# Optimization experiments

Hardware: AMD Instinct MI355X
Metric: run time of the kernel (lower is better)

## Reference

```python
import jax, jax.numpy as jnp
import numpy as np

DIM = 512
N_HEADS = 8
HEAD_DIM = DIM // N_HEADS
HID = 4 * DIM
N_LEVELS = 3  # len(chunk_sizes)
EPS = 1e-5


def layernorm(x, w, b):
    mu = jnp.mean(x, axis=-1, keepdims=True)
    var = jnp.var(x, axis=-1, keepdims=True)
    return (x - mu) * jax.lax.rsqrt(var + EPS) * w + b


def setup_inputs() -> dict:
    key = jax.random.key(0)
    ks = jax.random.split(key, 12)
    s = 1.0 / np.sqrt(DIM)
    sh = 1.0 / np.sqrt(HID)
    inp = {
        "x": jax.random.normal(ks[0], (4, 2048, DIM), dtype=jnp.float32),
        # torch nn.Linear stores weight as [out, in]; y = x @ W.T
        "Wq": jax.random.uniform(ks[1], (DIM, DIM), minval=-s, maxval=s),
        "Wk": jax.random.uniform(ks[2], (DIM, DIM), minval=-s, maxval=s),
        "Wv": jax.random.uniform(ks[3], (DIM, DIM), minval=-s, maxval=s),
        "Wo": jax.random.uniform(ks[4], (DIM, DIM), minval=-s, maxval=s),
        "ln1_w": jnp.ones((DIM,)), "ln1_b": jnp.zeros((DIM,)),
        "ln2_w": jnp.ones((DIM,)), "ln2_b": jnp.zeros((DIM,)),
        # CMS: per-level MLP, stored as [L, in, out]
        "cms_W1": jax.random.uniform(ks[5], (N_LEVELS, DIM, HID), minval=-s, maxval=s),
        "cms_b1": jnp.zeros((N_LEVELS, HID)),
        "cms_W2": jax.random.uniform(ks[6], (N_LEVELS, HID, DIM), minval=-sh, maxval=sh),
        "cms_b2": jnp.zeros((N_LEVELS, DIM)),
    }
    return inp


def self_mod_attn(h, Wq, Wk, Wv, Wo):
    B, S, _ = h.shape
    def split(y):  # [B,S,dim] -> [B,H,S,D]
        return y.reshape(B, S, N_HEADS, HEAD_DIM).transpose(0, 2, 1, 3)
    Q = split(h @ Wq.T)
    K = split(h @ Wk.T)
    V = split(h @ Wv.T)
    # per-step memory delta, mean over batch: U[h,s,d,k] = mean_b v_t k_t^T
    U = jnp.einsum("bhsd,bhsk->hsdk", V, K) / B
    # memory starts at zero (buffer) and accumulates INCLUDING step t before readout
    M = jnp.cumsum(U, axis=1)  # [H,S,D,D]
    y = jnp.einsum("hsdk,bhsk->bhsd", M, Q)  # readout
    y = y.transpose(0, 2, 1, 3).reshape(B, S, DIM)
    return y @ Wo.T


def cms(h, cms_W1, cms_b1, cms_W2, cms_b2):
    # sequential chain of per-level MLPs (dim -> 4*dim -> dim)
    for l in range(N_LEVELS):
        h = jax.nn.gelu(h @ cms_W1[l] + cms_b1[l]) @ cms_W2[l] + cms_b2[l]
    return h


def reference(x, Wq, Wk, Wv, Wo, ln1_w, ln1_b, ln2_w, ln2_b,
              cms_W1, cms_b1, cms_W2, cms_b2):
    x = x + self_mod_attn(layernorm(x, ln1_w, ln1_b), Wq, Wk, Wv, Wo)
    x = x + cms(layernorm(x, ln2_w, ln2_b), cms_W1, cms_b1, cms_W2, cms_b2)
    return x
```

## Files before the change

kernel.cpp:

```cpp
#include <hip/hip_runtime.h>
#include <hip/hip_bf16.h>
#include <cstdint>
#include <cstddef>

typedef __attribute__((ext_vector_type(8))) short bf16x8;
typedef __attribute__((ext_vector_type(4))) float f32x4;

#define MFMA16(a, b, c) __builtin_amdgcn_mfma_f32_16x16x32_bf16((a), (b), (c), 0, 0, 0)

static __device__ __forceinline__ unsigned short f2bf(float f) {
    union { float f; unsigned u; } v; v.f = f;
    unsigned r = v.u + 0x7fffu + ((v.u >> 16) & 1u);
    return (unsigned short)(r >> 16);
}

static __device__ __forceinline__ float bf2f(unsigned short u) {
    union { unsigned u; float f; } v; v.u = ((unsigned)u) << 16; return v.f;
}

static __device__ __forceinline__ float gelu_tanh(float x) {
    float z = 0.7978845608028654f * (x + 0.044715f * x * x * x);
    float a = fabsf(z);
    float e = __expf(-2.0f * a);
    float t = (1.0f - e) / (1.0f + e);
    t = (z < 0.0f) ? -t : t;
    return 0.5f * x * (1.0f + t);
}

static __device__ __forceinline__ void gload16(const void* g, void* l) {
    __builtin_amdgcn_global_load_lds((const __attribute__((address_space(1))) unsigned int*)g,
                                     (__attribute__((address_space(3))) unsigned int*)l,
                                     16, 0, 0);
}

__global__ __launch_bounds__(256) void wcvt_kernel(const float* __restrict__ a, const float* __restrict__ b,
                                                   const float* __restrict__ c, const float* __restrict__ d,
                                                   unsigned short* __restrict__ o) {
    int i = blockIdx.x * 256 + threadIdx.x;
    int idx = i * 4;
    int which = idx >> 18;
    int off = idx & 262143;
    const float* src = (which == 0) ? a : (which == 1) ? b : (which == 2) ? c : d;
    float4 v = *(const float4*)(src + off);
    unsigned long long p = (unsigned long long)f2bf(v.x) | ((unsigned long long)f2bf(v.y) << 16)
                         | ((unsigned long long)f2bf(v.z) << 32) | ((unsigned long long)f2bf(v.w) << 48);
    *(unsigned long long*)(o + idx) = p;
}

__global__ __launch_bounds__(256) void wtrans_kernel(const float* __restrict__ in, unsigned short* __restrict__ out,
                                                     int R, int C) {
    __shared__ float tile[32][33];
    size_t lvl = blockIdx.z;
    in  += lvl * (size_t)R * C;
    out += lvl * (size_t)R * C;
    int c0 = blockIdx.x * 32, r0 = blockIdx.y * 32;
    int tx = threadIdx.x & 31, ty = threadIdx.x >> 5;
    #pragma unroll
    for (int ii = 0; ii < 4; ++ii) {
        int i = ty * 4 + ii;
        tile[i][tx] = in[(size_t)(r0 + i) * C + c0 + tx];
    }
    __syncthreads();
    #pragma unroll
    for (int jj = 0; jj < 4; ++jj) {
        int j = ty * 4 + jj;
        out[(size_t)(c0 + j) * R + r0 + tx] = f2bf(tile[tx][j]);
    }
}

__global__ __launch_bounds__(256) void ln_kernel(const float* __restrict__ x,
                                                 const float* __restrict__ w,
                                                 const float* __restrict__ b,
                                                 unsigned short* __restrict__ out) {
    int tid = threadIdx.x, l = tid & 63, wv = tid >> 6;
    size_t row = (size_t)blockIdx.x * 4 + wv;
    const float* xr = x + row * 512 + l * 8;
    float4 v0 = *(const float4*)xr;
    float4 v1 = *(const float4*)(xr + 4);
    float vv[8] = {v0.x, v0.y, v0.z, v0.w, v1.x, v1.y, v1.z, v1.w};
    float s = 0.f, q = 0.f;
    #pragma unroll
    for (int j = 0; j < 8; ++j) { s += vv[j]; q += vv[j] * vv[j]; }
    #pragma unroll
    for (int off = 1; off < 64; off <<= 1) { s += __shfl_xor(s, off); q += __shfl_xor(q, off); }
    float mu = s * (1.0f / 512.0f);
    float rs = rsqrtf(q * (1.0f / 512.0f) - mu * mu + 1e-5f);
    union { unsigned short us[8]; uint4 u; } pk;
    #pragma unroll
    for (int j = 0; j < 8; ++j)
        pk.us[j] = f2bf((vv[j] - mu) * rs * w[l * 8 + j] + b[l * 8 + j]);
    *(uint4*)(out + row * 512 + l * 8) = pk.u;
}

template<int EPI>
__global__ __launch_bounds__(512, 2) void gemm256(
    const unsigned short* __restrict__ A,
    const unsigned short* __restrict__ Bt,
    int K, int lda, int ldb, int N,
    unsigned short* __restrict__ outb,
    const float* __restrict__ bias,
    size_t planeStride) {
    __shared__ bf16x8 As[2][2048];
    __shared__ bf16x8 Bs[2][2048];
    const int tid = threadIdx.x, l = tid & 63, w = tid >> 6;
    const int m0 = blockIdx.x * 256, n0 = blockIdx.y * 256;
    const int wr = (w >> 2) * 128, wc = (w & 3) * 64;
    const int srow = l >> 3;
    const int scol = ((l & 7) ^ srow) * 8;

    if constexpr (EPI == 5) {
        size_t z = blockIdx.z;
        A    += z * (size_t)K;
        Bt   += z * (size_t)K;
        outb += z * planeStride;
    }

    const int nkt = K >> 6;
    auto stage = [&](int buf, int kt) {
        const unsigned short* Ag = A + (size_t)m0 * lda + kt * 64;
        const unsigned short* Bg = Bt + (size_t)n0 * ldb + kt * 64;
        #pragma unroll
        for (int i = 0; i < 4; ++i) {
            int chunk = i * 8 + w;
            int row = chunk * 8 + srow;
            gload16(Ag + (size_t)row * lda + scol, &As[buf][chunk * 64]);
            gload16(Bg + (size_t)row * ldb + scol, &Bs[buf][chunk * 64]);
        }
    };

    f32x4 acc[8][4] = {};
    stage(0, 0);
    __syncthreads();
    int cur = 0;
    for (int kt = 0; kt < nkt; ++kt) {
        if (kt + 1 < nkt) stage(cur ^ 1, kt + 1);
        #pragma unroll
        for (int kk = 0; kk < 2; ++kk) {
            bf16x8 af[8], bfr[4];
            #pragma unroll
            for (int mi = 0; mi < 8; ++mi) {
                int r = wr + mi * 16 + (l & 15);
                af[mi] = As[cur][r * 8 + ((kk * 4 + (l >> 4)) ^ (r & 7))];
            }
            #pragma unroll
            for (int ni = 0; ni < 4; ++ni) {
                int r = wc + ni * 16 + (l & 15);
                bfr[ni] = Bs[cur][r * 8 + ((kk * 4 + (l >> 4)) ^ (r & 7))];
            }
            #pragma unroll
            for (int mi = 0; mi < 8; ++mi)
                #pragma unroll
                for (int ni = 0; ni < 4; ++ni)
                    acc[mi][ni] = MFMA16(af[mi], bfr[ni], acc[mi][ni]);
        }
        __syncthreads();
        cur ^= 1;
    }

    #pragma unroll
    for (int mi = 0; mi < 8; ++mi)
        #pragma unroll
        for (int ni = 0; ni < 4; ++ni) {
            int col = n0 + wc + ni * 16 + (l & 15);
            #pragma unroll
            for (int r = 0; r < 4; ++r) {
                int row = m0 + wr + mi * 16 + (l >> 4) * 4 + r;
                float v = acc[mi][ni][r];
                size_t idx = (size_t)row * N + col;
                if constexpr (EPI == 0) {
                    outb[idx] = f2bf(v);
                } else if constexpr (EPI == 2) {
                    v += bias[col];
                    outb[idx] = f2bf(gelu_tanh(v));
                } else {
                    outb[idx] = f2bf(v);
                }
            }
        }
}

template<int EPI, int TN>
__global__ __launch_bounds__(256) void gemm_bt(
    const unsigned short* __restrict__ A,
    const unsigned short* __restrict__ Bt,
    int K, int lda, int ldb, int N,
    unsigned short* __restrict__ outb,
    float* __restrict__ outf,
    const float* __restrict__ bias,
    const float* __restrict__ resid) {
    constexpr int NI = TN / 32;
    constexpr int BCH = TN / 32;
    __shared__ bf16x8 As[2][1024];
    __shared__ bf16x8 Bs[2][TN * 8];
    const int tid = threadIdx.x, l = tid & 63, w = tid >> 6;
    const int m0 = blockIdx.x * 128, n0 = blockIdx.y * TN;
    const int wr = (w >> 1) * 64, wc = (w & 1) * (TN / 2);
    const int srow = l >> 3;
    const int scol = ((l & 7) ^ srow) * 8;

    const int nkt = K >> 6;
    auto stage = [&](int buf, int kt) {
        const unsigned short* Ag = A + (size_t)m0 * lda + kt * 64;
        const unsigned short* Bg = Bt + (size_t)n0 * ldb + kt * 64;
        #pragma unroll
        for (int i = 0; i < 4; ++i) {
            int chunk = i * 4 + w;
            int row = chunk * 8 + srow;
            gload16(Ag + (size_t)row * lda + scol, &As[buf][chunk * 64]);
        }
        #pragma unroll
        for (int i = 0; i < BCH; ++i) {
            int chunk = i * 4 + w;
            int row = chunk * 8 + srow;
            gload16(Bg + (size_t)row * ldb + scol, &Bs[buf][chunk * 64]);
        }
    };

    f32x4 acc[4][NI] = {};
    stage(0, 0);
    __syncthreads();
    int cur = 0;
    for (int kt = 0; kt < nkt; ++kt) {
        if (kt + 1 < nkt) stage(cur ^ 1, kt + 1);
        #pragma unroll
        for (int kk = 0; kk < 2; ++kk) {
            bf16x8 af[4], bfr[NI];
            #pragma unroll
            for (int mi = 0; mi < 4; ++mi) {
                int r = wr + mi * 16 + (l & 15);
                af[mi] = As[cur][r * 8 + ((kk * 4 + (l >> 4)) ^ (r & 7))];
            }
            #pragma unroll
            for (int ni = 0; ni < NI; ++ni) {
                int r = wc + ni * 16 + (l & 15);
                bfr[ni] = Bs[cur][r * 8 + ((kk * 4 + (l >> 4)) ^ (r & 7))];
            }
            #pragma unroll
            for (int mi = 0; mi < 4; ++mi)
                #pragma unroll
                for (int ni = 0; ni < NI; ++ni)
                    acc[mi][ni] = MFMA16(af[mi], bfr[ni], acc[mi][ni]);
        }
        __syncthreads();
        cur ^= 1;
    }

    #pragma unroll
    for (int mi = 0; mi < 4; ++mi)
        #pragma unroll
        for (int ni = 0; ni < NI; ++ni) {
            int col = n0 + wc + ni * 16 + (l & 15);
            #pragma unroll
            for (int r = 0; r < 4; ++r) {
                int row = m0 + wr + mi * 16 + (l >> 4) * 4 + r;
                float v = acc[mi][ni][r];
                size_t idx = (size_t)row * N + col;
                if constexpr (EPI == 1) {
                    outf[idx] = v + resid[idx];
                } else {
                    outb[idx] = f2bf(v);
                }
            }
        }
}

template<bool FINAL>
__global__ __launch_bounds__(256) void reduce_down(const unsigned short* __restrict__ P,
                                                   const float* __restrict__ bias,
                                                   const float* __restrict__ resid,
                                                   unsigned short* __restrict__ outb,
                                                   float* __restrict__ outf) {
    size_t i = ((size_t)blockIdx.x * 256 + threadIdx.x) * 8;
    int col = (int)(i & 511);
    bf16x8 a0 = *(const bf16x8*)(P + i);
    bf16x8 a1 = *(const bf16x8*)(P + 4194304 + i);
    bf16x8 a2 = *(const bf16x8*)(P + 2 * 4194304 + i);
    bf16x8 a3 = *(const bf16x8*)(P + 3 * 4194304 + i);
    float4 b0 = *(const float4*)(bias + col);
    float4 b1 = *(const float4*)(bias + col + 4);
    float bs[8] = {b0.x, b0.y, b0.z, b0.w, b1.x, b1.y, b1.z, b1.w};
    float v[8];
    #pragma unroll
    for (int j = 0; j < 8; ++j)
        v[j] = (bf2f((unsigned short)a0[j]) + bf2f((unsigned short)a1[j]))
             + (bf2f((unsigned short)a2[j]) + bf2f((unsigned short)a3[j])) + bs[j];
    if constexpr (FINAL) {
        const float4 r0 = *(const float4*)(resid + i);
        const float4 r1 = *(const float4*)(resid + i + 4);
        float4 o0 = {v[0] + r0.x, v[1] + r0.y, v[2] + r0.z, v[3] + r0.w};
        float4 o1 = {v[4] + r1.x, v[5] + r1.y, v[6] + r1.z, v[7] + r1.w};
        *(float4*)(outf + i) = o0;
        *(float4*)(outf + i + 4) = o1;
    } else {
        union { unsigned short us[8]; uint4 u; } pk;
        #pragma unroll
        for (int j = 0; j < 8; ++j) pk.us[j] = f2bf(v[j]);
        *(uint4*)(outb + i) = pk.u;
    }
}

__global__ __launch_bounds__(256) void attn_u_kernel(
    const unsigned short* __restrict__ QKV,
    float* __restrict__ U) {
    const int c = blockIdx.x, h = blockIdx.y;
    const int tid = threadIdx.x, l = tid & 63, w = tid >> 6;
    __shared__ __align__(16) unsigned short Kt[64 * 256];
    __shared__ __align__(16) unsigned short Vt[64 * 256];
    for (int i = 0; i < 8; ++i) {
        int idx = i * 256 + tid;
        int tr = idx >> 3, g = idx & 7;
        int bb = tr >> 6, tl = tr & 63;
        size_t go = (size_t)(bb * 2048 + c * 64 + tl) * 1536 + h * 64 + g * 8;
        bf16x8 kv = *(const bf16x8*)(QKV + go + 512);
        bf16x8 vv = *(const bf16x8*)(QKV + go + 1024);
        #pragma unroll
        for (int j = 0; j < 8; ++j) {
            int d = g * 8 + j;
            int ts = tr ^ ((d & 7) << 3);
            Kt[d * 256 + ts] = (unsigned short)kv[j];
            Vt[d * 256 + ts] = (unsigned short)vv[j];
        }
    }
    __syncthreads();
    const int dr = (w >> 1) * 32, kc = (w & 1) * 32;
    f32x4 acc[2][2] = {};
    #pragma unroll
    for (int kk = 0; kk < 8; ++kk) {
        bf16x8 av[2], bk[2];
        #pragma unroll
        for (int mi = 0; mi < 2; ++mi) {
            int r = dr + mi * 16 + (l & 15);
            av[mi] = *(const bf16x8*)&Vt[r * 256 + ((kk * 32 + (l >> 4) * 8) ^ ((r & 7) << 3))];
        }
        #pragma unroll
        for (int ni = 0; ni < 2; ++ni) {
            int r = kc + ni * 16 + (l & 15);
            bk[ni] = *(const bf16x8*)&Kt[r * 256 + ((kk * 32 + (l >> 4) * 8) ^ ((r & 7) << 3))];
        }
        #pragma unroll
        for (int mi = 0; mi < 2; ++mi)
            #pragma unroll
            for (int ni = 0; ni < 2; ++ni)
                acc[mi][ni] = MFMA16(av[mi], bk[ni], acc[mi][ni]);
    }
    float* Uo = U + (size_t)(h * 32 + c) * 4096;
    #pragma unroll
    for (int mi = 0; mi < 2; ++mi)
        #pragma unroll
        for (int ni = 0; ni < 2; ++ni)
            #pragma unroll
            for (int r = 0; r < 4; ++r) {
                int d = dr + mi * 16 + (l >> 4) * 4 + r;
                int k2 = kc + ni * 16 + (l & 15);
                Uo[d * 64 + k2] = acc[mi][ni][r] * 0.25f;
            }
}

__global__ __launch_bounds__(256) void attn_scan_kernel(const float* __restrict__ U,
                                                        unsigned short* __restrict__ Mx) {
    int e = blockIdx.x * 256 + threadIdx.x;
    int h = blockIdx.y;
    const float* Ub = U + (size_t)h * 32 * 4096 + e;
    unsigned short* Mb = Mx + (size_t)h * 32 * 4096 + e;
    float a = 0.0f;
    #pragma unroll
    for (int c0 = 0; c0 < 32; c0 += 4) {
        float u0 = Ub[(c0 + 0) * 4096];
        float u1 = Ub[(c0 + 1) * 4096];
        float u2 = Ub[(c0 + 2) * 4096];
        float u3 = Ub[(c0 + 3) * 4096];
        Mb[(c0 + 0) * 4096] = f2bf(a); a += u0;
        Mb[(c0 + 1) * 4096] = f2bf(a); a += u1;
        Mb[(c0 + 2) * 4096] = f2bf(a); a += u2;
        Mb[(c0 + 3) * 4096] = f2bf(a); a += u3;
    }
}

__global__ __launch_bounds__(256) void attn_y_kernel(
    const unsigned short* __restrict__ QKV,
    const unsigned short* __restrict__ Mx,
    unsigned short* __restrict__ Y) {
    const int c = blockIdx.x, h = blockIdx.y;
    const int tid = threadIdx.x, l = tid & 63, w = tid >> 6;
    __shared__ __align__(16) unsigned short Vt[64 * 256];
    __shared__ __align__(16) unsigned short Ss[4][64 * 64];

    for (int i = 0; i < 8; ++i) {
        int idx = i * 256 + tid;
        int tr = idx >> 3, g = idx & 7;
        int bb = tr >> 6, tl = tr & 63;
        bf16x8 vv = *(const bf16x8*)(QKV + ((size_t)(bb * 2048 + c * 64 + tl) * 1536 + 1024 + h * 64 + g * 8));
        #pragma unroll
        for (int j = 0; j < 8; ++j) {
            int d = g * 8 + j;
            Vt[d * 256 + (tr ^ ((d & 7) << 3))] = (unsigned short)vv[j];
        }
    }
    __syncthreads();

    f32x4 yacc[4][4] = {};

    bf16x8 qf[2][4];
    #pragma unroll
    for (int kk = 0; kk < 2; ++kk)
        #pragma unroll
        for (int ni = 0; ni < 4; ++ni) {
            int qloc = ni * 16 + (l & 15);
            qf[kk][ni] = *(const bf16x8*)(QKV + ((size_t)(w * 2048 + c * 64 + qloc) * 1536
                                                + h * 64 + kk * 32 + (l >> 4) * 8));
        }

    const unsigned short* Mrow = Mx + (size_t)(h * 32 + c) * 4096;
    #pragma unroll
    for (int kk = 0; kk < 2; ++kk) {
        bf16x8 am[4];
        #pragma unroll
        for (int mi = 0; mi < 4; ++mi) {
            int d = mi * 16 + (l & 15);
            am[mi] = *(const bf16x8*)(Mrow + d * 64 + kk * 32 + (l >> 4) * 8);
        }
        #pragma unroll
        for (int mi = 0; mi < 4; ++mi)
            #pragma unroll
            for (int ni = 0; ni < 4; ++ni)
                yacc[mi][ni] = MFMA16(am[mi], qf[kk][ni], yacc[mi][ni]);
    }

    unsigned short* Sw = &Ss[w][0];
    for (int tv = 0; tv < 4; ++tv) {
        #pragma unroll
        for (int th = 0; th < 2; ++th) {
            f32x4 sacc[2][4] = {};
            #pragma unroll
            for (int kk = 0; kk < 2; ++kk) {
                bf16x8 ak[2];
                #pragma unroll
                for (int mi = 0; mi < 2; ++mi) {
                    int tloc = th * 32 + mi * 16 + (l & 15);
                    ak[mi] = *(const bf16x8*)(QKV + ((size_t)(tv * 2048 + c * 64 + tloc) * 1536
                                                    + 512 + h * 64 + kk * 32 + (l >> 4) * 8));
                }
                #pragma unroll
                for (int mi = 0; mi < 2; ++mi)
                    #pragma unroll
                    for (int ni = 0; ni < 4; ++ni)
                        sacc[mi][ni] = MFMA16(ak[mi], qf[kk][ni], sacc[mi][ni]);
            }
            #pragma unroll
            for (int mi = 0; mi < 2; ++mi)
                #pragma unroll
                for (int ni = 0; ni < 4; ++ni) {
                    int tb = th * 32 + mi * 16 + (l >> 4) * 4;
                    int qcol = ni * 16 + (l & 15);
                    unsigned long long p = 0;
                    #pragma unroll
                    for (int r = 0; r < 4; ++r) {
                        float v = (tb + r <= qcol) ? sacc[mi][ni][r] * 0.25f : 0.0f;
                        p |= ((unsigned long long)f2bf(v)) << (16 * r);
                    }
                    int ts = tb ^ ((qcol & 7) << 3);
                    *(unsigned long long*)(Sw + qcol * 64 + ts) = p;
                }
        }
        #pragma unroll
        for (int kk2 = 0; kk2 < 2; ++kk2) {
            bf16x8 av[4], bs[4];
            #pragma unroll
            for (int mi = 0; mi < 4; ++mi) {
                int d = mi * 16 + (l & 15);
                av[mi] = *(const bf16x8*)&Vt[d * 256 + ((tv * 64 + kk2 * 32 + (l >> 4) * 8) ^ ((d & 7) << 3))];
            }
            #pragma unroll
            for (int ni = 0; ni < 4; ++ni) {
                int q = ni * 16 + (l & 15);
                bs[ni] = *(const bf16x8*)&Sw[q * 64 + ((kk2 * 32 + (l >> 4) * 8) ^ ((q & 7) << 3))];
            }
            #pragma unroll
            for (int mi = 0; mi < 4; ++mi)
                #pragma unroll
                for (int ni = 0; ni < 4; ++ni)
                    yacc[mi][ni] = MFMA16(av[mi], bs[ni], yacc[mi][ni]);
        }
    }

    #pragma unroll
    for (int mi = 0; mi < 4; ++mi)
        #pragma unroll
        for (int ni = 0; ni < 4; ++ni) {
            int qloc = ni * 16 + (l & 15);
            int d0 = mi * 16 + (l >> 4) * 4;
            unsigned long long p = 0;
            #pragma unroll
            for (int r = 0; r < 4; ++r)
                p |= ((unsigned long long)f2bf(yacc[mi][ni][r])) << (16 * r);
            *(unsigned long long*)(Y + ((size_t)(w * 2048 + c * 64 + qloc) * 512 + h * 64 + d0)) = p;
        }
}

extern "C" void kernel_launch(void* const* d_in, const int* in_sizes, int n_in,
                              void* d_out, int out_size, void* d_ws, size_t ws_size,
                              hipStream_t stream) {
    const float* x    = (const float*)d_in[0];
    const float* Wq   = (const float*)d_in[1];
    const float* Wk   = (const float*)d_in[2];
    const float* Wv   = (const float*)d_in[3];
    const float* Wo   = (const float*)d_in[4];
    const float* ln1w = (const float*)d_in[5];
    const float* ln1b = (const float*)d_in[6];
    const float* ln2w = (const float*)d_in[7];
    const float* ln2b = (const float*)d_in[8];
    const float* W1   = (const float*)d_in[9];
    const float* b1   = (const float*)d_in[10];
    const float* W2   = (const float*)d_in[11];
    const float* b2   = (const float*)d_in[12];
    float* out = (float*)d_out;
    char* ws = (char*)d_ws;
    const size_t MB = 1024 * 1024;
    unsigned short* Wqb  = (unsigned short*)(ws + 0 * MB);
    unsigned short* W1t  = (unsigned short*)(ws + 2 * MB);
    unsigned short* W2t  = (unsigned short*)(ws + 8 * MB);
    unsigned short* hb   = (unsigned short*)(ws + 14 * MB);
    unsigned short* QKVb = (unsigned short*)(ws + 22 * MB);
    unsigned short* Yb   = (unsigned short*)(ws + 46 * MB);
    unsigned short* tb   = (unsigned short*)(ws + 22 * MB);
    float*          x2   = (float*)(ws + 54 * MB);
    float*          U    = (float*)(ws + 70 * MB);
    unsigned short* Mx   = (unsigned short*)(ws + 74 * MB);
    unsigned short* P    = (unsigned short*)(ws + 76 * MB);

    const bool splitk = ws_size >= (size_t)108 * MB;

    wcvt_kernel<<<1024, 256, 0, stream>>>(Wq, Wk, Wv, Wo, Wqb);
    wtrans_kernel<<<dim3(64, 16, 3), 256, 0, stream>>>(W1, W1t, 512, 2048);
    wtrans_kernel<<<dim3(16, 64, 3), 256, 0, stream>>>(W2, W2t, 2048, 512);

    ln_kernel<<<2048, 256, 0, stream>>>(x, ln1w, ln1b, hb);

    gemm256<0><<<dim3(32, 6), 512, 0, stream>>>(hb, Wqb, 512, 512, 512, 1536,
                                                QKVb, nullptr, 0);

    attn_u_kernel<<<dim3(32, 8), 256, 0, stream>>>(QKVb, U);
    attn_scan_kernel<<<dim3(16, 8), 256, 0, stream>>>(U, Mx);
    attn_y_kernel<<<dim3(32, 8), 256, 0, stream>>>(QKVb, Mx, Yb);

    gemm_bt<1, 128><<<dim3(64, 4), 256, 0, stream>>>(Yb, Wqb + 3 * 262144, 512, 512, 512, 512,
                                                     nullptr, x2, nullptr, x);

    ln_kernel<<<2048, 256, 0, stream>>>(x2, ln2w, ln2b, hb);

    for (int lvl = 0; lvl < 3; ++lvl) {
        gemm256<2><<<dim3(32, 8), 512, 0, stream>>>(hb, W1t + (size_t)lvl * 1048576,
                                                    512, 512, 512, 2048,
                                                    tb, b1 + lvl * 2048, 0);
        if (splitk) {
            gemm256<5><<<dim3(32, 2, 4), 512, 0, stream>>>(tb, W2t + (size_t)lvl * 1048576,
                                                           512, 2048, 2048, 512,
                                                           P, nullptr, (size_t)8192 * 512);
            if (lvl < 2)
                reduce_down<false><<<2048, 256, 0, stream>>>(P, b2 + lvl * 512, nullptr, hb, nullptr);
            else
                reduce_down<true><<<2048, 256, 0, stream>>>(P, b2 + lvl * 512, x2, nullptr, out);
        } else {
            gemm256<5><<<dim3(32, 2, 1), 512, 0, stream>>>(tb, W2t + (size_t)lvl * 1048576,
                                                           2048, 2048, 2048, 512,
                                                           P, nullptr, 0);
            if (lvl < 2)
                reduce_down<false><<<2048, 256, 0, stream>>>(P, b2 + lvl * 512, nullptr, hb, nullptr);
            else
                reduce_down<true><<<2048, 256, 0, stream>>>(P, b2 + lvl * 512, x2, nullptr, out);
        }
    }
}
```

Measured before the change: 281.1 us.

## Interleave GEMM main loop into quadrant phases with split staging and priority

Restructures the 256x256 bf16 GEMM main loop into four quadrant MFMA phases. Each phase is preceded by partial LDS fragment loads and one half of the next tile's A or B global-to-LDS staging. Raw s_barrier, sched_barrier, explicit vmcnt waits and s_setprio replace the single __syncthreads, so global loads overlap MFMA work at finer grain. The intent is to hide load latency and cut register pressure from holding full fragments. The cost is more barriers per k-tile and reliance on hand-counted vmcnt values, which could be wrong and cause data races.

```diff
diff --git a/kernel.cpp b/kernel.cpp
--- a/kernel.cpp
+++ b/kernel.cpp
@@ -7,6 +7,8 @@
 typedef __attribute__((ext_vector_type(4))) float f32x4;
 
 #define MFMA16(a, b, c) __builtin_amdgcn_mfma_f32_16x16x32_bf16((a), (b), (c), 0, 0, 0)
+#define SBAR()  __builtin_amdgcn_s_barrier()
+#define SCHED0() __builtin_amdgcn_sched_barrier(0)
 
 static __device__ __forceinline__ unsigned short f2bf(float f) {
     union { float f; unsigned u; } v; v.f = f;
@@ -116,44 +118,122 @@
     }
 
     const int nkt = K >> 6;
-    auto stage = [&](int buf, int kt) {
+
+    auto stageA = [&](int buf, int kt, int h) {
         const unsigned short* Ag = A + (size_t)m0 * lda + kt * 64;
-        const unsigned short* Bg = Bt + (size_t)n0 * ldb + kt * 64;
-        #pragma unroll
-        for (int i = 0; i < 4; ++i) {
-            int chunk = i * 8 + w;
+        #pragma unroll
+        for (int i = 0; i < 2; ++i) {
+            int chunk = h * 8 + i * 16 + w;
             int row = chunk * 8 + srow;
             gload16(Ag + (size_t)row * lda + scol, &As[buf][chunk * 64]);
+        }
+    };
+    auto stageB = [&](int buf, int kt, int h) {
+        const unsigned short* Bg = Bt + (size_t)n0 * ldb + kt * 64;
+        #pragma unroll
+        for (int i = 0; i < 2; ++i) {
+            int chunk = ((i * 2 + (w >> 2)) << 3) | (h << 2) | (w & 3);
+            int row = chunk * 8 + srow;
             gload16(Bg + (size_t)row * ldb + scol, &Bs[buf][chunk * 64]);
         }
     };
 
     f32x4 acc[8][4] = {};
-    stage(0, 0);
-    __syncthreads();
+
+    stageB(0, 0, 0); stageB(0, 0, 1); stageA(0, 0, 0); stageA(0, 0, 1);
+    asm volatile("s_waitcnt vmcnt(2)" ::: "memory");
+    SBAR(); SCHED0();
+
     int cur = 0;
     for (int kt = 0; kt < nkt; ++kt) {
-        if (kt + 1 < nkt) stage(cur ^ 1, kt + 1);
-        #pragma unroll
-        for (int kk = 0; kk < 2; ++kk) {
-            bf16x8 af[8], bfr[4];
-            #pragma unroll
-            for (int mi = 0; mi < 8; ++mi) {
-                int r = wr + mi * 16 + (l & 15);
-                af[mi] = As[cur][r * 8 + ((kk * 4 + (l >> 4)) ^ (r & 7))];
-            }
-            #pragma unroll
-            for (int ni = 0; ni < 4; ++ni) {
-                int r = wc + ni * 16 + (l & 15);
-                bfr[ni] = Bs[cur][r * 8 + ((kk * 4 + (l >> 4)) ^ (r & 7))];
-            }
-            #pragma unroll
-            for (int mi = 0; mi < 8; ++mi)
-                #pragma unroll
-                for (int ni = 0; ni < 4; ++ni)
-                    acc[mi][ni] = MFMA16(af[mi], bfr[ni], acc[mi][ni]);
-        }
-        __syncthreads();
+        const bool more = (kt + 1 < nkt);
+        bf16x8 af[4][2], bf_lo[2][2], bf_hi[2][2];
+
+        #pragma unroll
+        for (int mi = 0; mi < 4; ++mi) {
+            int r = wr + mi * 16 + (l & 15);
+            #pragma unroll
+            for (int kk = 0; kk < 2; ++kk)
+                af[mi][kk] = As[cur][r * 8 + ((kk * 4 + (l >> 4)) ^ (r & 7))];
+        }
+        #pragma unroll
+        for (int ni = 0; ni < 2; ++ni) {
+            int r = wc + ni * 16 + (l & 15);
+            #pragma unroll
+            for (int kk = 0; kk < 2; ++kk)
+                bf_lo[ni][kk] = Bs[cur][r * 8 + ((kk * 4 + (l >> 4)) ^ (r & 7))];
+        }
+        if (more) stageB(cur ^ 1, kt + 1, 0);
+        SBAR(); SCHED0();
+        __builtin_amdgcn_s_setprio(1);
+        #pragma unroll
+        for (int mi = 0; mi < 4; ++mi)
+            #pragma unroll
+            for (int ni = 0; ni < 2; ++ni)
+                #pragma unroll
+                for (int kk = 0; kk < 2; ++kk)
+                    acc[mi][ni] = MFMA16(af[mi][kk], bf_lo[ni][kk], acc[mi][ni]);
+        __builtin_amdgcn_s_setprio(0);
+        SCHED0(); SBAR();
+
+        #pragma unroll
+        for (int ni = 0; ni < 2; ++ni) {
+            int r = wc + (2 + ni) * 16 + (l & 15);
+            #pragma unroll
+            for (int kk = 0; kk < 2; ++kk)
+                bf_hi[ni][kk] = Bs[cur][r * 8 + ((kk * 4 + (l >> 4)) ^ (r & 7))];
+        }
+        if (more) stageB(cur ^ 1, kt + 1, 1);
+        SBAR(); SCHED0();
+        __builtin_amdgcn_s_setprio(1);
+        #pragma unroll
+        for (int mi = 0; mi < 4; ++mi)
+            #pragma unroll
+            for (int ni = 0; ni < 2; ++ni)
+                #pragma unroll
+                for (int kk = 0; kk < 2; ++kk)
+                    acc[mi][2 + ni] = MFMA16(af[mi][kk], bf_hi[ni][kk], acc[mi][2 + ni]);
+        __builtin_amdgcn_s_setprio(0);
+        SCHED0();
+        if (more) asm volatile("s_waitcnt vmcnt(4)" ::: "memory");
+        else      asm volatile("s_waitcnt vmcnt(0)" ::: "memory");
+        SBAR(); SCHED0();
+
+        #pragma unroll
+        for (int mi = 0; mi < 4; ++mi) {
+            int r = wr + 64 + mi * 16 + (l & 15);
+            #pragma unroll
+            for (int kk = 0; kk < 2; ++kk)
+                af[mi][kk] = As[cur][r * 8 + ((kk * 4 + (l >> 4)) ^ (r & 7))];
+        }
+        if (more) stageA(cur ^ 1, kt + 1, 0);
+        SBAR(); SCHED0();
+        __builtin_amdgcn_s_setprio(1);
+        #pragma unroll
+        for (int mi = 0; mi < 4; ++mi)
+            #pragma unroll
+            for (int ni = 0; ni < 2; ++ni)
+                #pragma unroll
+                for (int kk = 0; kk < 2; ++kk)
+                    acc[4 + mi][ni] = MFMA16(af[mi][kk], bf_lo[ni][kk], acc[4 + mi][ni]);
+        __builtin_amdgcn_s_setprio(0);
+        SCHED0(); SBAR();
+
+        if (more) stageA(cur ^ 1, kt + 1, 1);
+        SBAR(); SCHED0();
+        __builtin_amdgcn_s_setprio(1);
+        #pragma unroll
+        for (int mi = 0; mi < 4; ++mi)
+            #pragma unroll
+            for (int ni = 0; ni < 2; ++ni)
+                #pragma unroll
+                for (int kk = 0; kk < 2; ++kk)
+                    acc[4 + mi][2 + ni] = MFMA16(af[mi][kk], bf_hi[ni][kk], acc[4 + mi][2 + ni]);
+        __builtin_amdgcn_s_setprio(0);
+        SCHED0();
+        if (more) asm volatile("s_waitcnt vmcnt(2)" ::: "memory");
+        SBAR(); SCHED0();
+
         cur ^= 1;
     }
 
```

Result: no change. 280.3 us (-0.3%).
